# Optimization experiments

Measured on AMD Instinct MI355X. Metric: run time of the kernel, lower is better.

Reference implementation:

```python
import jax, jax.numpy as jnp
import numpy as np

DT = 0.01          # discretization timestep (init kwarg dt)
DAMP_MIN = 5e-4    # minimum damping (init kwarg damp_min)
BATCH, SEQ, D_IN, N_STATE = 16, 2048, 1024, 128


def setup_inputs() -> dict:
    key = jax.random.key(0)
    k1, k2, k3, k4, k5 = jax.random.split(key, 5)
    u = jax.random.normal(k1, (BATCH, SEQ, D_IN), jnp.float32)
    # A_real init: randn*0.1 - damp_min, then clamped to <= -damp_min (stability)
    A_real = jnp.minimum(jax.random.normal(k2, (N_STATE,), jnp.float32) * 0.1 - DAMP_MIN, -DAMP_MIN)
    A_imag = jax.random.normal(k3, (N_STATE,), jnp.float32)
    B = jax.random.normal(k4, (N_STATE, D_IN), jnp.float32) * 0.02
    C = jax.random.normal(k5, (D_IN, N_STATE), jnp.float32) * 0.02
    return {"u": u, "A_real": A_real, "A_imag": A_imag, "B": B, "C": C}


def reference(u, A_real, A_imag, B, C):
    """Real-input path of StableResonantSSM.

    Bilinear discretization of diagonal complex A:
      a_disc = (1 + dt/2 * a) / (1 - dt/2 * a)          (elementwise, A diagonal)
      B_disc = sqrt(dt) * B / (1 - dt/2 * a)            (row-wise scaling)
    Recurrence: h_t = a_disc * h_{t-1} + B_disc @ u_t;  y_t = Re(C @ h_t).
    """
    dt = jnp.float32(DT)
    a = (A_real + 1j * A_imag).astype(jnp.complex64)          # (N,)
    denom = 1.0 - (dt / 2) * a                                 # (N,) complex
    a_disc = (1.0 + (dt / 2) * a) / denom                      # (N,)
    B_disc = (jnp.sqrt(dt) * B.astype(jnp.complex64)) / denom[:, None]  # (N, D)

    # Precompute all input injections as one GEMM: (T, B, N) complex
    Bu = jnp.einsum('btd,nd->tbn', u, B_disc)

    def step(h, bu_t):
        h = a_disc * h + bu_t
        return h, h

    h0 = jnp.zeros((u.shape[0], a.shape[0]), jnp.complex64)
    _, hs = jax.lax.scan(step, h0, Bu)                         # hs: (T, B, N)

    # C is real, so Re(C @ h) == C @ Re(h)
    y = jnp.einsum('tbn,dn->btd', hs.real, C)                  # (B, T, D)
    return y
```

## Files before the change

### kernel.cpp

```cpp
#include <hip/hip_runtime.h>
#include <hip/hip_bf16.h>
#include <cstdint>

#define DT_F    0.01f
#define NB      16
#define T_SEQ   2048
#define DD      1024
#define NS      128
#define CHUNK   64
#define NCH     32

using f32x4  = __attribute__((ext_vector_type(4))) float;
using bf16x8 = __attribute__((ext_vector_type(8))) short;
using fl4    = __attribute__((ext_vector_type(4))) float;

#define AS1(p) ((const __attribute__((address_space(1))) void*)(p))
#define AS3(p) ((__attribute__((address_space(3))) void*)(p))

__device__ __forceinline__ unsigned short f2bf(float f) {
  union { float f; unsigned u; } v; v.f = f;
  unsigned r = v.u + 0x7fffu + ((v.u >> 16) & 1u);
  return (unsigned short)(r >> 16);
}
__device__ __forceinline__ float bf2f(unsigned short s) {
  union { unsigned u; float f; } v; v.u = ((unsigned)s) << 16;
  return v.f;
}
__device__ __forceinline__ unsigned short f2bf_hw(float f) {
  __hip_bfloat16 h = __float2bfloat16(f);
  return __builtin_bit_cast(unsigned short, h);
}

__device__ __forceinline__ void adisc(float Arn, float Ain, float& ar, float& ai) {
  const float dr = 1.f - 0.5f * DT_F * Arn;
  const float di = -0.5f * DT_F * Ain;
  const float inv = 1.f / (dr * dr + di * di);
  const float nr = 1.f + 0.5f * DT_F * Arn;
  const float nim = 0.5f * DT_F * Ain;
  ar = (nr * dr + nim * di) * inv;
  ai = (nim * dr - nr * di) * inv;
}

__global__ void prep_all(const float* __restrict__ Ar, const float* __restrict__ Ai,
                         const float* __restrict__ B, const float* __restrict__ C,
                         unsigned short* __restrict__ W, unsigned short* __restrict__ Cb) {
  const int blk = blockIdx.x;
  const int tid = threadIdx.x;
  if (blk < 512) {
    const int i = blk * 256 + tid;
    Cb[i] = f2bf(C[i]);
    return;
  }
  const int n = blk - 512;
  const float ar = Ar[n], ai = Ai[n];
  const float dr = 1.f - 0.5f * DT_F * ar;
  const float di = -0.5f * DT_F * ai;
  const float inv = 1.f / (dr * dr + di * di);
  const float s  = sqrtf(DT_F);
  const float cr = s * dr * inv;
  const float ci = -s * di * inv;
  for (int d = tid; d < DD; d += 256) {
    const float b = B[(size_t)n * DD + d];
    W[(size_t)n * DD + d]        = f2bf(b * cr);
    W[(size_t)(NS + n) * DD + d] = f2bf(b * ci);
  }
}

__global__ __launch_bounds__(256, 2) void gemm1s(const float* __restrict__ U,
                                                 const float* __restrict__ Ar,
                                                 const float* __restrict__ Ai,
                                                 const unsigned short* __restrict__ W,
                                                 unsigned short* __restrict__ Hs,
                                                 float* __restrict__ F) {
  __shared__ __align__(16) char smem[40960];
  unsigned short* As = (unsigned short*)smem;
  unsigned short* Bs = (unsigned short*)(smem + 8192);
  char*           Bt = smem;

  const int tid  = threadIdx.x;
  const int lane = tid & 63;
  const int wave = tid >> 6;
  const int blk  = blockIdx.x;
  const size_t m0 = (size_t)blk * CHUNK;

  f32x4 acc[4][4];
  const f32x4 zero = {0.f, 0.f, 0.f, 0.f};
#pragma unroll
  for (int i = 0; i < 4; ++i)
#pragma unroll
    for (int j = 0; j < 4; ++j) acc[i][j] = zero;

  const int srow  = tid >> 2;
  const int scol  = (tid & 3) * 16;
  const int growl = lane >> 3;
  const int gcol  = (lane & 7) * 8;

  for (int k0 = 0; k0 < DD; k0 += 64) {
    __syncthreads();
#pragma unroll
    for (int g = 0; g < 8; ++g) {
      const int row = wave * 64 + g * 8;
      const unsigned short* gb = W + (size_t)(row + growl) * DD + k0 + gcol;
      __builtin_amdgcn_global_load_lds(AS1(gb), AS3(&Bs[row * 64]), 16, 0, 0);
    }
    {
      const float* ga = U + (m0 + srow) * DD + k0 + scol;
      fl4 v0 = *(const fl4*)ga;
      fl4 v1 = *(const fl4*)(ga + 4);
      fl4 v2 = *(const fl4*)(ga + 8);
      fl4 v3 = *(const fl4*)(ga + 12);
      bf16x8 p0, p1;
#pragma unroll
      for (int e = 0; e < 4; ++e) {
        p0[e] = (short)f2bf_hw(v0[e]); p0[4 + e] = (short)f2bf_hw(v1[e]);
        p1[e] = (short)f2bf_hw(v2[e]); p1[4 + e] = (short)f2bf_hw(v3[e]);
      }
      *(bf16x8*)&As[srow * 64 + scol]     = p0;
      *(bf16x8*)&As[srow * 64 + scol + 8] = p1;
    }
    __syncthreads();
#pragma unroll
    for (int ks = 0; ks < 2; ++ks) {
      bf16x8 af[4], bfr[4];
#pragma unroll
      for (int i = 0; i < 4; ++i)
        af[i] = *(const bf16x8*)&As[(i * 16 + (lane & 15)) * 64 + ks * 32 + (lane >> 4) * 8];
#pragma unroll
      for (int j = 0; j < 4; ++j)
        bfr[j] = *(const bf16x8*)&Bs[(wave * 64 + j * 16 + (lane & 15)) * 64 + ks * 32 + (lane >> 4) * 8];
#pragma unroll
      for (int i = 0; i < 4; ++i)
#pragma unroll
        for (int j = 0; j < 4; ++j)
          acc[i][j] = __builtin_amdgcn_mfma_f32_16x16x32_bf16(af[i], bfr[j], acc[i][j], 0, 0, 0);
    }
  }
  __syncthreads();

#pragma unroll
  for (int i = 0; i < 4; ++i) {
#pragma unroll
    for (int j = 0; j < 4; ++j) {
      const int cc = wave * 64 + j * 16 + (lane & 15);
#pragma unroll
      for (int q = 0; q < 4; ++q) {
        const int t = i * 16 + (lane >> 4) * 4 + q;
        *(unsigned short*)(Bt + t * 512 + ((cc * 2) ^ ((t & 7) << 4))) = f2bf_hw(acc[i][j][q]);
      }
    }
  }
  __syncthreads();

  if (tid < 128) {
    const int n = tid;
    float ar, ai; adisc(Ar[n], Ai[n], ar, ai);
    float hr = 0.f, hi = 0.f;
    unsigned short* o = Hs + (size_t)blk * (CHUNK * NS) + n;
#pragma unroll 8
    for (int t = 0; t < CHUNK; ++t) {
      const int reByte = t * 512 + ((n * 2) ^ ((t & 7) << 4));
      const float br = bf2f(*(const unsigned short*)(Bt + reByte));
      const float bi = bf2f(*(const unsigned short*)(Bt + reByte + 256));
      const float xr = fmaf(ar, hr, fmaf(-ai, hi, br));
      const float xi = fmaf(ar, hi, fmaf(ai, hr, bi));
      hr = xr; hi = xi;
      o[t * NS] = f2bf(hr);
    }
    F[(size_t)blk * 256 + n]       = hr;
    F[(size_t)blk * 256 + 128 + n] = hi;
  }
}

__global__ __launch_bounds__(256, 2) void gemm2s(const unsigned short* __restrict__ Hs,
                                                 const float* __restrict__ F,
                                                 const float* __restrict__ Ar,
                                                 const float* __restrict__ Ai,
                                                 const unsigned short* __restrict__ Cb,
                                                 float* __restrict__ y) {
  __shared__ __align__(16) char Hl[64 * 256];
  const int tid  = threadIdx.x;
  const int lane = tid & 63;
  const int wave = tid >> 6;
  const int blk  = blockIdx.x;
  const int c    = blk & 31;
  const size_t m0 = (size_t)blk * CHUNK;

  const char* tile = (const char*)Hs + (size_t)blk * (CHUNK * NS * 2);
#pragma unroll
  for (int g = 0; g < 4; ++g) {
    const int r0 = wave * 16 + g * 4;
    const int r  = r0 + (lane >> 4);
    const int srcOff = r * 256 + ((((lane & 15)) * 16) ^ ((r & 7) << 4));
    __builtin_amdgcn_global_load_lds(AS1(tile + srcOff), AS3(Hl + r0 * 256), 16, 0, 0);
  }
  __syncthreads();

  if (tid < 128) {
    const int n = tid;
    float ar, ai; adisc(Ar[n], Ai[n], ar, ai);
    if (c != 0) {
      float alr = ar, ali = ai;
#pragma unroll
      for (int s = 0; s < 6; ++s) {
        const float tr = alr * alr - ali * ali;
        const float ti = 2.f * alr * ali;
        alr = tr; ali = ti;
      }
      float cr = 0.f, ci = 0.f;
      const float* Fb = F + (size_t)(blk - c) * 256;
      for (int cc = 0; cc < c; ++cc) {
        const float fr = Fb[(size_t)cc * 256 + n];
        const float fi = Fb[(size_t)cc * 256 + 128 + n];
        const float xr = fmaf(alr, cr, fmaf(-ali, ci, fr));
        const float xi = fmaf(alr, ci, fmaf(ali, cr, fi));
        cr = xr; ci = xi;
      }
      float gr = ar * cr - ai * ci;
      float gi = ar * ci + ai * cr;
#pragma unroll 8
      for (int t = 0; t < CHUNK; ++t) {
        unsigned short* pp = (unsigned short*)(Hl + t * 256 + ((n * 2) ^ ((t & 7) << 4)));
        *pp = f2bf(bf2f(*pp) + gr);
        const float xr = ar * gr - ai * gi;
        const float xi = ar * gi + ai * gr;
        gr = xr; gi = xi;
      }
    }
  }
  __syncthreads();

  const f32x4 zero = {0.f, 0.f, 0.f, 0.f};
#pragma unroll
  for (int cg = 0; cg < 4; ++cg) {
    const int d0 = wave * 256 + cg * 64;
    f32x4 oacc[4][4];
#pragma unroll
    for (int i = 0; i < 4; ++i)
#pragma unroll
      for (int j = 0; j < 4; ++j) oacc[i][j] = zero;

#pragma unroll
    for (int ks = 0; ks < 4; ++ks) {
      bf16x8 af[4], bfr[4];
#pragma unroll
      for (int i = 0; i < 4; ++i) {
        const int r = i * 16 + (lane & 15);
        af[i] = *(const bf16x8*)(Hl + r * 256 + ((ks * 64 + (lane >> 4) * 16) ^ ((r & 7) << 4)));
      }
#pragma unroll
      for (int j = 0; j < 4; ++j)
        bfr[j] = *(const bf16x8*)(Cb + (size_t)(d0 + j * 16 + (lane & 15)) * NS + ks * 32 + (lane >> 4) * 8);
#pragma unroll
      for (int i = 0; i < 4; ++i)
#pragma unroll
        for (int j = 0; j < 4; ++j)
          oacc[i][j] = __builtin_amdgcn_mfma_f32_16x16x32_bf16(af[i], bfr[j], oacc[i][j], 0, 0, 0);
    }
#pragma unroll
    for (int i = 0; i < 4; ++i) {
      const size_t r0 = m0 + i * 16 + (lane >> 4) * 4;
#pragma unroll
      for (int j = 0; j < 4; ++j) {
        const int d = d0 + j * 16 + (lane & 15);
#pragma unroll
        for (int q = 0; q < 4; ++q)
          y[(r0 + q) * DD + d] = oacc[i][j][q];
      }
    }
  }
}

extern "C" void kernel_launch(void* const* d_in, const int* in_sizes, int n_in,
                              void* d_out, int out_size, void* d_ws, size_t ws_size,
                              hipStream_t stream) {
  const float* u  = (const float*)d_in[0];
  const float* Ar = (const float*)d_in[1];
  const float* Ai = (const float*)d_in[2];
  const float* B  = (const float*)d_in[3];
  const float* C  = (const float*)d_in[4];
  float* y = (float*)d_out;
  char* ws = (char*)d_ws;

  unsigned short* W  = (unsigned short*)(ws);
  unsigned short* Cb = (unsigned short*)(ws + (512 << 10));
  float*          F  = (float*)(ws + (768 << 10));
  unsigned short* Hs = (unsigned short*)(ws + (1280 << 10));

  prep_all<<<dim3(640), dim3(256), 0, stream>>>(Ar, Ai, B, C, W, Cb);
  gemm1s<<<dim3(NB * NCH), dim3(256), 0, stream>>>(u, Ar, Ai, W, Hs, F);
  gemm2s<<<dim3(NB * NCH), dim3(256), 0, stream>>>(Hs, F, Ar, Ai, Cb, y);
}
```

Measured before the change: 84.02 us.

## Double-buffer W tiles and prefetch U into registers in gemm1s K-loop

Restructures the gemm1s K-loop into a software pipeline. The next W tile is loaded asynchronously into a second LDS buffer and the next U slice is prefetched into registers while the MFMAs run on the current tile. U is converted to bf16 and written to LDS after a barrier. The intent is to hide global-load latency behind compute. The cost is LDS growing from 40KB to 72KB per block, which may reduce occupancy below the launch_bounds target of 2 blocks per CU, and there is a subtle synchronisation around the async LDS loads.

```diff
diff --git a/kernel.cpp b/kernel.cpp
--- a/kernel.cpp
+++ b/kernel.cpp
@@ -72,10 +72,11 @@
                                                  const unsigned short* __restrict__ W,
                                                  unsigned short* __restrict__ Hs,
                                                  float* __restrict__ F) {
-  __shared__ __align__(16) char smem[40960];
-  unsigned short* As = (unsigned short*)smem;
-  unsigned short* Bs = (unsigned short*)(smem + 8192);
-  char*           Bt = smem;
+  __shared__ __align__(16) char smem[73728];
+  unsigned short* As  = (unsigned short*)smem;
+  unsigned short* Bs0 = (unsigned short*)(smem + 8192);
+  unsigned short* Bs1 = (unsigned short*)(smem + 8192 + 32768);
+  char*           Bt  = smem;
 
   const int tid  = threadIdx.x;
   const int lane = tid & 63;
@@ -95,30 +96,47 @@
   const int growl = lane >> 3;
   const int gcol  = (lane & 7) * 8;
 
-  for (int k0 = 0; k0 < DD; k0 += 64) {
-    __syncthreads();
+  {
+    const float* ga = U + (m0 + srow) * DD + scol;
+    fl4 v0 = *(const fl4*)ga;
+    fl4 v1 = *(const fl4*)(ga + 4);
+    fl4 v2 = *(const fl4*)(ga + 8);
+    fl4 v3 = *(const fl4*)(ga + 12);
 #pragma unroll
     for (int g = 0; g < 8; ++g) {
       const int row = wave * 64 + g * 8;
-      const unsigned short* gb = W + (size_t)(row + growl) * DD + k0 + gcol;
-      __builtin_amdgcn_global_load_lds(AS1(gb), AS3(&Bs[row * 64]), 16, 0, 0);
-    }
-    {
-      const float* ga = U + (m0 + srow) * DD + k0 + scol;
-      fl4 v0 = *(const fl4*)ga;
-      fl4 v1 = *(const fl4*)(ga + 4);
-      fl4 v2 = *(const fl4*)(ga + 8);
-      fl4 v3 = *(const fl4*)(ga + 12);
-      bf16x8 p0, p1;
-#pragma unroll
-      for (int e = 0; e < 4; ++e) {
-        p0[e] = (short)f2bf_hw(v0[e]); p0[4 + e] = (short)f2bf_hw(v1[e]);
-        p1[e] = (short)f2bf_hw(v2[e]); p1[4 + e] = (short)f2bf_hw(v3[e]);
-      }
-      *(bf16x8*)&As[srow * 64 + scol]     = p0;
-      *(bf16x8*)&As[srow * 64 + scol + 8] = p1;
-    }
-    __syncthreads();
+      const unsigned short* gb = W + (size_t)(row + growl) * DD + gcol;
+      __builtin_amdgcn_global_load_lds(AS1(gb), AS3(&Bs0[row * 64]), 16, 0, 0);
+    }
+    bf16x8 q0, q1;
+#pragma unroll
+    for (int e = 0; e < 4; ++e) {
+      q0[e] = (short)f2bf_hw(v0[e]); q0[4 + e] = (short)f2bf_hw(v1[e]);
+      q1[e] = (short)f2bf_hw(v2[e]); q1[4 + e] = (short)f2bf_hw(v3[e]);
+    }
+    *(bf16x8*)&As[srow * 64 + scol]     = q0;
+    *(bf16x8*)&As[srow * 64 + scol + 8] = q1;
+  }
+  __syncthreads();
+
+  fl4 p0, p1, p2, p3;
+  for (int t = 0; t < 16; ++t) {
+    unsigned short* Bcur = (t & 1) ? Bs1 : Bs0;
+    unsigned short* Bnxt = (t & 1) ? Bs0 : Bs1;
+    if (t < 15) {
+      const int k1 = (t + 1) * 64;
+      const float* ga = U + (m0 + srow) * DD + k1 + scol;
+      p0 = *(const fl4*)ga;
+      p1 = *(const fl4*)(ga + 4);
+      p2 = *(const fl4*)(ga + 8);
+      p3 = *(const fl4*)(ga + 12);
+#pragma unroll
+      for (int g = 0; g < 8; ++g) {
+        const int row = wave * 64 + g * 8;
+        const unsigned short* gb = W + (size_t)(row + growl) * DD + k1 + gcol;
+        __builtin_amdgcn_global_load_lds(AS1(gb), AS3(&Bnxt[row * 64]), 16, 0, 0);
+      }
+    }
 #pragma unroll
     for (int ks = 0; ks < 2; ++ks) {
       bf16x8 af[4], bfr[4];
@@ -127,12 +145,25 @@
         af[i] = *(const bf16x8*)&As[(i * 16 + (lane & 15)) * 64 + ks * 32 + (lane >> 4) * 8];
 #pragma unroll
       for (int j = 0; j < 4; ++j)
-        bfr[j] = *(const bf16x8*)&Bs[(wave * 64 + j * 16 + (lane & 15)) * 64 + ks * 32 + (lane >> 4) * 8];
+        bfr[j] = *(const bf16x8*)&Bcur[(wave * 64 + j * 16 + (lane & 15)) * 64 + ks * 32 + (lane >> 4) * 8];
 #pragma unroll
       for (int i = 0; i < 4; ++i)
 #pragma unroll
         for (int j = 0; j < 4; ++j)
           acc[i][j] = __builtin_amdgcn_mfma_f32_16x16x32_bf16(af[i], bfr[j], acc[i][j], 0, 0, 0);
+    }
+    if (t < 15) {
+      __builtin_amdgcn_s_barrier();
+      __builtin_amdgcn_sched_barrier(0);
+      bf16x8 q0, q1;
+#pragma unroll
+      for (int e = 0; e < 4; ++e) {
+        q0[e] = (short)f2bf_hw(p0[e]); q0[4 + e] = (short)f2bf_hw(p1[e]);
+        q1[e] = (short)f2bf_hw(p2[e]); q1[4 + e] = (short)f2bf_hw(p3[e]);
+      }
+      *(bf16x8*)&As[srow * 64 + scol]     = q0;
+      *(bf16x8*)&As[srow * 64 + scol + 8] = q1;
+      __syncthreads();
     }
   }
   __syncthreads();
```

Result: no change. 84.48 us (+0.6%).

## Fuse chunk scan and output GEMM into one kernel with inter-block flag sync

Applied to the files above, without the earlier changes.

Merges the input-GEMM/local-scan kernel and the carry-fixup/output-GEMM kernel into one. Local states stay in LDS instead of a bf16 global round trip, and each block waits on per-chunk release/acquire flags for earlier chunks' final states before applying the carry. This removes one launch plus the Hs write and reload. It relies on all earlier blocks being resident or already scheduled: 512 blocks at 2 per CU fit on MI355X, but the code does not enforce this, so a spin deadlock is possible if residency fails.

```diff
diff --git a/kernel.cpp b/kernel.cpp
--- a/kernel.cpp
+++ b/kernel.cpp
@@ -43,10 +43,13 @@
 
 __global__ void prep_all(const float* __restrict__ Ar, const float* __restrict__ Ai,
                          const float* __restrict__ B, const float* __restrict__ C,
-                         unsigned short* __restrict__ W, unsigned short* __restrict__ Cb) {
+                         unsigned short* __restrict__ W, unsigned short* __restrict__ Cb,
+                         int* __restrict__ flags) {
   const int blk = blockIdx.x;
   const int tid = threadIdx.x;
   if (blk < 512) {
+    if (blk < 2)
+      __hip_atomic_store(&flags[blk * 256 + tid], 0, __ATOMIC_RELAXED, __HIP_MEMORY_SCOPE_AGENT);
     const int i = blk * 256 + tid;
     Cb[i] = f2bf(C[i]);
     return;
@@ -66,12 +69,14 @@
   }
 }
 
-__global__ __launch_bounds__(256, 2) void gemm1s(const float* __restrict__ U,
-                                                 const float* __restrict__ Ar,
-                                                 const float* __restrict__ Ai,
-                                                 const unsigned short* __restrict__ W,
-                                                 unsigned short* __restrict__ Hs,
-                                                 float* __restrict__ F) {
+__global__ __launch_bounds__(256, 2) void fused(const float* __restrict__ U,
+                                                const float* __restrict__ Ar,
+                                                const float* __restrict__ Ai,
+                                                const unsigned short* __restrict__ W,
+                                                const unsigned short* __restrict__ Cb,
+                                                float* __restrict__ F,
+                                                int* __restrict__ flags,
+                                                float* __restrict__ y) {
   __shared__ __align__(16) char smem[40960];
   unsigned short* As = (unsigned short*)smem;
   unsigned short* Bs = (unsigned short*)(smem + 8192);
@@ -81,6 +86,7 @@
   const int lane = tid & 63;
   const int wave = tid >> 6;
   const int blk  = blockIdx.x;
+  const int c    = blk & 31;
   const size_t m0 = (size_t)blk * CHUNK;
 
   f32x4 acc[4][4];
@@ -155,7 +161,6 @@
     const int n = tid;
     float ar, ai; adisc(Ar[n], Ai[n], ar, ai);
     float hr = 0.f, hi = 0.f;
-    unsigned short* o = Hs + (size_t)blk * (CHUNK * NS) + n;
 #pragma unroll 8
     for (int t = 0; t < CHUNK; ++t) {
       const int reByte = t * 512 + ((n * 2) ^ ((t & 7) << 4));
@@ -164,41 +169,28 @@
       const float xr = fmaf(ar, hr, fmaf(-ai, hi, br));
       const float xi = fmaf(ar, hi, fmaf(ai, hr, bi));
       hr = xr; hi = xi;
-      o[t * NS] = f2bf(hr);
-    }
-    F[(size_t)blk * 256 + n]       = hr;
-    F[(size_t)blk * 256 + 128 + n] = hi;
-  }
-}
-
-__global__ __launch_bounds__(256, 2) void gemm2s(const unsigned short* __restrict__ Hs,
-                                                 const float* __restrict__ F,
-                                                 const float* __restrict__ Ar,
-                                                 const float* __restrict__ Ai,
-                                                 const unsigned short* __restrict__ Cb,
-                                                 float* __restrict__ y) {
-  __shared__ __align__(16) char Hl[64 * 256];
-  const int tid  = threadIdx.x;
-  const int lane = tid & 63;
-  const int wave = tid >> 6;
-  const int blk  = blockIdx.x;
-  const int c    = blk & 31;
-  const size_t m0 = (size_t)blk * CHUNK;
-
-  const char* tile = (const char*)Hs + (size_t)blk * (CHUNK * NS * 2);
-#pragma unroll
-  for (int g = 0; g < 4; ++g) {
-    const int r0 = wave * 16 + g * 4;
-    const int r  = r0 + (lane >> 4);
-    const int srcOff = r * 256 + ((((lane & 15)) * 16) ^ ((r & 7) << 4));
-    __builtin_amdgcn_global_load_lds(AS1(tile + srcOff), AS3(Hl + r0 * 256), 16, 0, 0);
+      *(unsigned short*)(Bt + reByte) = f2bf(hr);
+    }
+    __hip_atomic_store(&F[(size_t)blk * 256 + n],       hr, __ATOMIC_RELAXED, __HIP_MEMORY_SCOPE_AGENT);
+    __hip_atomic_store(&F[(size_t)blk * 256 + 128 + n], hi, __ATOMIC_RELAXED, __HIP_MEMORY_SCOPE_AGENT);
   }
   __syncthreads();
-
-  if (tid < 128) {
-    const int n = tid;
-    float ar, ai; adisc(Ar[n], Ai[n], ar, ai);
-    if (c != 0) {
+  if (tid == 0)
+    __hip_atomic_store(&flags[blk], 1, __ATOMIC_RELEASE, __HIP_MEMORY_SCOPE_AGENT);
+
+  if (c != 0) {
+    if (tid == 0) {
+      const int base = blk - c;
+      for (int cc = 0; cc < c; ++cc) {
+        while (__hip_atomic_load(&flags[base + cc], __ATOMIC_ACQUIRE, __HIP_MEMORY_SCOPE_AGENT) == 0)
+          __builtin_amdgcn_s_sleep(2);
+      }
+    }
+    __syncthreads();
+
+    if (tid < 128) {
+      const int n = tid;
+      float ar, ai; adisc(Ar[n], Ai[n], ar, ai);
       float alr = ar, ali = ai;
 #pragma unroll
       for (int s = 0; s < 6; ++s) {
@@ -209,8 +201,8 @@
       float cr = 0.f, ci = 0.f;
       const float* Fb = F + (size_t)(blk - c) * 256;
       for (int cc = 0; cc < c; ++cc) {
-        const float fr = Fb[(size_t)cc * 256 + n];
-        const float fi = Fb[(size_t)cc * 256 + 128 + n];
+        const float fr = __hip_atomic_load(&Fb[(size_t)cc * 256 + n],       __ATOMIC_RELAXED, __HIP_MEMORY_SCOPE_AGENT);
+        const float fi = __hip_atomic_load(&Fb[(size_t)cc * 256 + 128 + n], __ATOMIC_RELAXED, __HIP_MEMORY_SCOPE_AGENT);
         const float xr = fmaf(alr, cr, fmaf(-ali, ci, fr));
         const float xi = fmaf(alr, ci, fmaf(ali, cr, fi));
         cr = xr; ci = xi;
@@ -219,17 +211,16 @@
       float gi = ar * ci + ai * cr;
 #pragma unroll 8
       for (int t = 0; t < CHUNK; ++t) {
-        unsigned short* pp = (unsigned short*)(Hl + t * 256 + ((n * 2) ^ ((t & 7) << 4)));
+        unsigned short* pp = (unsigned short*)(Bt + t * 512 + ((n * 2) ^ ((t & 7) << 4)));
         *pp = f2bf(bf2f(*pp) + gr);
         const float xr = ar * gr - ai * gi;
         const float xi = ar * gi + ai * gr;
         gr = xr; gi = xi;
       }
     }
-  }
-  __syncthreads();
-
-  const f32x4 zero = {0.f, 0.f, 0.f, 0.f};
+    __syncthreads();
+  }
+
 #pragma unroll
   for (int cg = 0; cg < 4; ++cg) {
     const int d0 = wave * 256 + cg * 64;
@@ -245,7 +236,7 @@
 #pragma unroll
       for (int i = 0; i < 4; ++i) {
         const int r = i * 16 + (lane & 15);
-        af[i] = *(const bf16x8*)(Hl + r * 256 + ((ks * 64 + (lane >> 4) * 16) ^ ((r & 7) << 4)));
+        af[i] = *(const bf16x8*)(Bt + r * 512 + ((ks * 64 + (lane >> 4) * 16) ^ ((r & 7) << 4)));
       }
 #pragma unroll
       for (int j = 0; j < 4; ++j)
@@ -281,12 +272,11 @@
   float* y = (float*)d_out;
   char* ws = (char*)d_ws;
 
-  unsigned short* W  = (unsigned short*)(ws);
-  unsigned short* Cb = (unsigned short*)(ws + (512 << 10));
-  float*          F  = (float*)(ws + (768 << 10));
-  unsigned short* Hs = (unsigned short*)(ws + (1280 << 10));
-
-  prep_all<<<dim3(640), dim3(256), 0, stream>>>(Ar, Ai, B, C, W, Cb);
-  gemm1s<<<dim3(NB * NCH), dim3(256), 0, stream>>>(u, Ar, Ai, W, Hs, F);
-  gemm2s<<<dim3(NB * NCH), dim3(256), 0, stream>>>(Hs, F, Ar, Ai, Cb, y);
-}
+  unsigned short* W     = (unsigned short*)(ws);
+  unsigned short* Cb    = (unsigned short*)(ws + (512 << 10));
+  float*          F     = (float*)(ws + (768 << 10));
+  int*            flags = (int*)(ws + (1280 << 10));
+
+  prep_all<<<dim3(640), dim3(256), 0, stream>>>(Ar, Ai, B, C, W, Cb, flags);
+  fused<<<dim3(NB * NCH), dim3(256), 0, stream>>>(u, Ar, Ai, W, Cb, F, flags, y);
+}
```

New measurement: 147.1 us. 1.75x slower.
